# Optimization experiments

Measured on AMD Instinct MI355X. Metric: run time of the kernel, lower is better.

## Reference

```python
import jax, jax.numpy as jnp
import numpy as np

N_NODES = 50000
N_EDGES = 800000
D_IN = 128
D_OUT = 128


def setup_inputs() -> dict:
    key = jax.random.key(0)
    ks = jax.random.split(key, 10)
    x = jax.random.normal(ks[0], (N_NODES, D_IN), dtype=jnp.float32)
    lp_rows = jax.random.randint(ks[1], (N_EDGES,), 0, N_NODES, dtype=jnp.int32)
    lp_cols = jax.random.randint(ks[2], (N_EDGES,), 0, N_NODES, dtype=jnp.int32)
    # low-pass operator: positive normalized-adjacency-like weights
    lp_vals = jax.random.uniform(ks[3], (N_EDGES,), dtype=jnp.float32) / 16.0
    hp_rows = jax.random.randint(ks[4], (N_EDGES,), 0, N_NODES, dtype=jnp.int32)
    hp_cols = jax.random.randint(ks[5], (N_EDGES,), 0, N_NODES, dtype=jnp.int32)
    # high-pass operator: signed (Laplacian-like) weights
    hp_vals = jax.random.normal(ks[6], (N_EDGES,), dtype=jnp.float32) / 16.0
    alpha_w = jax.random.normal(ks[7], (1, D_IN), dtype=jnp.float32) * 0.05
    alpha_b = jnp.zeros((1,), dtype=jnp.float32)
    W = jax.random.normal(ks[8], (D_OUT, D_IN), dtype=jnp.float32) * (1.0 / np.sqrt(D_IN))
    b = jnp.zeros((D_OUT,), dtype=jnp.float32)
    return {"x": x, "lp_rows": lp_rows, "lp_cols": lp_cols, "lp_vals": lp_vals,
            "hp_rows": hp_rows, "hp_cols": hp_cols, "hp_vals": hp_vals,
            "alpha_w": alpha_w, "alpha_b": alpha_b, "W": W, "b": b}


def _spmm(rows, cols, vals, x, n):
    # COO sparse-dense matmul: out[r] += vals[e] * x[cols[e]]
    return jax.ops.segment_sum(vals[:, None] * x[cols], rows, num_segments=n)


def reference(x, lp_rows, lp_cols, lp_vals, hp_rows, hp_cols, hp_vals,
              alpha_w, alpha_b, W, b):
    n = x.shape[0]
    # per-node mixing gate: alpha_i = sigmoid(x_i . theta + b)  -> [N, 1]
    alpha = jax.nn.sigmoid(x @ alpha_w.T + alpha_b)
    z_lp = _spmm(lp_rows, lp_cols, lp_vals, x, n)   # [N, D_IN]
    z_hp = _spmm(hp_rows, hp_cols, hp_vals, x, n)   # [N, D_IN]
    z_mix = alpha * z_lp + (1.0 - alpha) * z_hp
    out = jax.nn.relu(z_mix @ W.T + b)              # use_activation=True
    return out, alpha
```

## Files before the change

kernel.cpp:

```cpp
#include <hip/hip_runtime.h>

#define N_NODES_C 50000
#define N_EDGES_C 800000
#define N_EDGES2_C (2 * N_EDGES_C)
#define D 128
#define CAP 128

static __device__ __forceinline__ unsigned short f2bf(float f) {
  unsigned u = __float_as_uint(f);
  u += 0x7fff + ((u >> 16) & 1);
  return (unsigned short)(u >> 16);
}
static __device__ __forceinline__ float bf_lo(unsigned u) {
  return __uint_as_float(u << 16);
}
static __device__ __forceinline__ float bf_hi(unsigned u) {
  return __uint_as_float(u & 0xffff0000u);
}

__global__ __launch_bounds__(256) void alpha_kernel(
    const float* __restrict__ x,
    const float* __restrict__ aw,
    const float* __restrict__ ab,
    float* __restrict__ alpha_out,
    float* __restrict__ alpha_ws,
    int n) {
  int wave = (int)((blockIdx.x * blockDim.x + threadIdx.x) >> 6);
  int lane = threadIdx.x & 63;
  if (wave >= n) return;
  const float* xr = x + (size_t)wave * D;
  float s = xr[lane] * aw[lane] + xr[lane + 64] * aw[lane + 64];
  #pragma unroll
  for (int off = 32; off > 0; off >>= 1)
    s += __shfl_down(s, off);
  if (lane == 0) {
    float a = 1.0f / (1.0f + __expf(-(s + ab[0])));
    alpha_out[wave] = a;
    alpha_ws[wave] = a;
  }
}

__global__ __launch_bounds__(256) void fill_kernel(
    const int* __restrict__ lp_rows, const int* __restrict__ lp_cols,
    const float* __restrict__ lp_vals,
    const int* __restrict__ hp_rows, const int* __restrict__ hp_cols,
    const float* __restrict__ hp_vals,
    const float* __restrict__ alpha,
    int* __restrict__ rcursor,
    unsigned* __restrict__ pairs) {
  int e = blockIdx.x * 256 + threadIdx.x;
  if (e >= N_EDGES2_C) return;
  int r, c;
  float v;
  if (e < N_EDGES_C) {
    r = lp_rows[e];
    c = lp_cols[e];
    v = lp_vals[e] * alpha[r];
  } else {
    int i = e - N_EDGES_C;
    r = hp_rows[i];
    c = hp_cols[i];
    v = hp_vals[i] * (1.0f - alpha[r]);
  }
  unsigned pk = (unsigned)c | ((unsigned)f2bf(v) << 16);
  int p = atomicAdd(&rcursor[r], 1);
  if (p < CAP) pairs[((size_t)r << 7) + p] = pk;
}

#define GNODES 64
#define GP 16
#define LDP 132

__global__ __launch_bounds__(256) void gemm_y_kernel(
    const float* __restrict__ x,
    const float* __restrict__ W,
    unsigned* __restrict__ y,
    int n) {
  __shared__ float wt[D][LDP];
  __shared__ float zs[GP][LDP];

  int t = threadIdx.x;
  int node0 = blockIdx.x * GNODES;

  #pragma unroll
  for (int it = 0; it < 16; ++it) {
    int f = t + it * 256;
    int j = f >> 5;
    int k4 = f & 31;
    *(float4*)&wt[j][k4 * 4] = ((const float4*)W)[f];
  }

  int tj = t & 31;
  int ns = t >> 5;
  int j0 = tj * 2;

  for (int p = 0; p < 4; ++p) {
    int nb = node0 + p * GP;
    __syncthreads();
    #pragma unroll
    for (int it = 0; it < 2; ++it) {
      int f = t + it * 256;
      int r = f >> 5;
      int c4 = f & 31;
      int node = nb + r;
      float4 v = make_float4(0.f, 0.f, 0.f, 0.f);
      if (node < n) v = ((const float4*)(x + (size_t)node * D))[c4];
      *(float4*)&zs[r][c4 * 4] = v;
    }
    __syncthreads();

    float acc[2][4] = {};
    #pragma unroll 4
    for (int k = 0; k < D; k += 4) {
      float4 w0 = *(const float4*)&wt[j0][k];
      float4 w1 = *(const float4*)&wt[j0 + 1][k];
      float4 w2 = *(const float4*)&wt[j0 + 64][k];
      float4 w3 = *(const float4*)&wt[j0 + 65][k];
      float4 z0 = *(const float4*)&zs[ns * 2 + 0][k];
      float4 z1 = *(const float4*)&zs[ns * 2 + 1][k];
      acc[0][0] += z0.x * w0.x + z0.y * w0.y + z0.z * w0.z + z0.w * w0.w;
      acc[0][1] += z0.x * w1.x + z0.y * w1.y + z0.z * w1.z + z0.w * w1.w;
      acc[0][2] += z0.x * w2.x + z0.y * w2.y + z0.z * w2.z + z0.w * w2.w;
      acc[0][3] += z0.x * w3.x + z0.y * w3.y + z0.z * w3.z + z0.w * w3.w;
      acc[1][0] += z1.x * w0.x + z1.y * w0.y + z1.z * w0.z + z1.w * w0.w;
      acc[1][1] += z1.x * w1.x + z1.y * w1.y + z1.z * w1.z + z1.w * w1.w;
      acc[1][2] += z1.x * w2.x + z1.y * w2.y + z1.z * w2.z + z1.w * w2.w;
      acc[1][3] += z1.x * w3.x + z1.y * w3.y + z1.z * w3.z + z1.w * w3.w;
    }

    #pragma unroll
    for (int ii = 0; ii < 2; ++ii) {
      int node = nb + ns * 2 + ii;
      if (node < n) {
        uint2 o;
        o.x = (unsigned)f2bf(acc[ii][0]) | ((unsigned)f2bf(acc[ii][2]) << 16);
        o.y = (unsigned)f2bf(acc[ii][1]) | ((unsigned)f2bf(acc[ii][3]) << 16);
        *(uint2*)&y[(size_t)node * 64 + j0] = o;
      }
    }
  }
}

__global__ __launch_bounds__(256) void gather_kernel(
    const int* __restrict__ rcursor,
    const unsigned* __restrict__ pairs,
    const unsigned* __restrict__ y,
    const float* __restrict__ bias,
    float* __restrict__ out) {
  int row = (int)((blockIdx.x * blockDim.x + threadIdx.x) >> 6);
  int lane = threadIdx.x & 63;
  if (row >= N_NODES_C) return;
  int deg = rcursor[row];
  if (deg > CAP) deg = CAP;
  const unsigned* pp = pairs + ((size_t)row << 7);
  float aL = 0.f, aH = 0.f;
  int p = 0;
  for (; p + 3 < deg; p += 4) {
    unsigned e0 = pp[p + 0];
    unsigned e1 = pp[p + 1];
    unsigned e2 = pp[p + 2];
    unsigned e3 = pp[p + 3];
    unsigned u0 = y[(size_t)(e0 & 0xffffu) * 64 + lane];
    unsigned u1 = y[(size_t)(e1 & 0xffffu) * 64 + lane];
    unsigned u2 = y[(size_t)(e2 & 0xffffu) * 64 + lane];
    unsigned u3 = y[(size_t)(e3 & 0xffffu) * 64 + lane];
    float v0 = bf_hi(e0);
    float v1 = bf_hi(e1);
    float v2 = bf_hi(e2);
    float v3 = bf_hi(e3);
    aL += v0 * bf_lo(u0) + v1 * bf_lo(u1) + v2 * bf_lo(u2) + v3 * bf_lo(u3);
    aH += v0 * bf_hi(u0) + v1 * bf_hi(u1) + v2 * bf_hi(u2) + v3 * bf_hi(u3);
  }
  for (; p < deg; ++p) {
    unsigned e0 = pp[p];
    unsigned u0 = y[(size_t)(e0 & 0xffffu) * 64 + lane];
    float v0 = bf_hi(e0);
    aL += v0 * bf_lo(u0);
    aH += v0 * bf_hi(u0);
  }
  out[(size_t)row * D + lane] = fmaxf(aL + bias[lane], 0.0f);
  out[(size_t)row * D + lane + 64] = fmaxf(aH + bias[lane + 64], 0.0f);
}

extern "C" void kernel_launch(void* const* d_in, const int* in_sizes, int n_in,
                              void* d_out, int out_size, void* d_ws, size_t ws_size,
                              hipStream_t stream) {
  const float* x = (const float*)d_in[0];
  const int* lp_rows = (const int*)d_in[1];
  const int* lp_cols = (const int*)d_in[2];
  const float* lp_vals = (const float*)d_in[3];
  const int* hp_rows = (const int*)d_in[4];
  const int* hp_cols = (const int*)d_in[5];
  const float* hp_vals = (const float*)d_in[6];
  const float* alpha_w = (const float*)d_in[7];
  const float* alpha_b = (const float*)d_in[8];
  const float* W = (const float*)d_in[9];
  const float* bias = (const float*)d_in[10];

  float* out = (float*)d_out;
  float* alpha_out = out + (size_t)N_NODES_C * D;

  char* ws = (char*)d_ws;
  unsigned* y = (unsigned*)ws;           ws += (size_t)N_NODES_C * 64 * 4;
  float* alpha_ws = (float*)ws;          ws += 200192;
  int* rcursor = (int*)ws;               ws += 200192;
  unsigned* pairs = (unsigned*)ws;
  ws += (size_t)N_NODES_C * CAP * 4;

  hipMemsetAsync(rcursor, 0, N_NODES_C * sizeof(int), stream);

  alpha_kernel<<<(N_NODES_C + 3) / 4, 256, 0, stream>>>(
      x, alpha_w, alpha_b, alpha_out, alpha_ws, N_NODES_C);

  fill_kernel<<<(N_EDGES2_C + 255) / 256, 256, 0, stream>>>(
      lp_rows, lp_cols, lp_vals, hp_rows, hp_cols, hp_vals,
      alpha_ws, rcursor, pairs);

  gemm_y_kernel<<<(N_NODES_C + GNODES - 1) / GNODES, 256, 0, stream>>>(
      x, W, y, N_NODES_C);

  gather_kernel<<<(N_NODES_C * 64 + 255) / 256, 256, 0, stream>>>(
      rcursor, pairs, (const unsigned*)y, bias, out);
}
```

Measured before the change: 307.6 us.

## Shard per-row edge buckets by XCD to localize atomic counters

The fill kernel now keeps eight per-row cursors and bucket segments, one per XCD, chosen by reading the hardware XCC id. The goal is to keep atomicAdd traffic on each row's counter within a single XCD's L2 and avoid cross-die coherence contention. The gather kernel walks all eight shards per row, adding loop overhead and doubling the pairs buffer footprint. Each shard holds at most 32 entries, so a heavily skewed distribution within one row could drop edges where the old 128-entry cap would not have.

```diff
diff --git a/kernel.cpp b/kernel.cpp
--- a/kernel.cpp
+++ b/kernel.cpp
@@ -4,7 +4,8 @@
 #define N_EDGES_C 800000
 #define N_EDGES2_C (2 * N_EDGES_C)
 #define D 128
-#define CAP 128
+#define NSHARD 8
+#define SCAP 32
 
 static __device__ __forceinline__ unsigned short f2bf(float f) {
   unsigned u = __float_as_uint(f);
@@ -16,6 +17,12 @@
 }
 static __device__ __forceinline__ float bf_hi(unsigned u) {
   return __uint_as_float(u & 0xffff0000u);
+}
+
+static __device__ __forceinline__ int xcd_id() {
+  int v;
+  asm volatile("s_getreg_b32 %0, hwreg(HW_REG_XCC_ID, 0, 4)" : "=s"(v));
+  return v & (NSHARD - 1);
 }
 
 __global__ __launch_bounds__(256) void alpha_kernel(
@@ -50,6 +57,7 @@
     unsigned* __restrict__ pairs) {
   int e = blockIdx.x * 256 + threadIdx.x;
   if (e >= N_EDGES2_C) return;
+  int xcc = xcd_id();
   int r, c;
   float v;
   if (e < N_EDGES_C) {
@@ -63,8 +71,8 @@
     v = hp_vals[i] * (1.0f - alpha[r]);
   }
   unsigned pk = (unsigned)c | ((unsigned)f2bf(v) << 16);
-  int p = atomicAdd(&rcursor[r], 1);
-  if (p < CAP) pairs[((size_t)r << 7) + p] = pk;
+  int p = atomicAdd(&rcursor[(r << 3) + xcc], 1);
+  if (p < SCAP) pairs[((size_t)r << 8) + (xcc << 5) + p] = pk;
 }
 
 #define GNODES 64
@@ -150,33 +158,38 @@
   int row = (int)((blockIdx.x * blockDim.x + threadIdx.x) >> 6);
   int lane = threadIdx.x & 63;
   if (row >= N_NODES_C) return;
-  int deg = rcursor[row];
-  if (deg > CAP) deg = CAP;
-  const unsigned* pp = pairs + ((size_t)row << 7);
+  const unsigned* pp = pairs + ((size_t)row << 8);
+  const int* cc = rcursor + (row << 3);
   float aL = 0.f, aH = 0.f;
-  int p = 0;
-  for (; p + 3 < deg; p += 4) {
-    unsigned e0 = pp[p + 0];
-    unsigned e1 = pp[p + 1];
-    unsigned e2 = pp[p + 2];
-    unsigned e3 = pp[p + 3];
-    unsigned u0 = y[(size_t)(e0 & 0xffffu) * 64 + lane];
-    unsigned u1 = y[(size_t)(e1 & 0xffffu) * 64 + lane];
-    unsigned u2 = y[(size_t)(e2 & 0xffffu) * 64 + lane];
-    unsigned u3 = y[(size_t)(e3 & 0xffffu) * 64 + lane];
-    float v0 = bf_hi(e0);
-    float v1 = bf_hi(e1);
-    float v2 = bf_hi(e2);
-    float v3 = bf_hi(e3);
-    aL += v0 * bf_lo(u0) + v1 * bf_lo(u1) + v2 * bf_lo(u2) + v3 * bf_lo(u3);
-    aH += v0 * bf_hi(u0) + v1 * bf_hi(u1) + v2 * bf_hi(u2) + v3 * bf_hi(u3);
-  }
-  for (; p < deg; ++p) {
-    unsigned e0 = pp[p];
-    unsigned u0 = y[(size_t)(e0 & 0xffffu) * 64 + lane];
-    float v0 = bf_hi(e0);
-    aL += v0 * bf_lo(u0);
-    aH += v0 * bf_hi(u0);
+  #pragma unroll
+  for (int s = 0; s < NSHARD; ++s) {
+    int deg = cc[s];
+    if (deg > SCAP) deg = SCAP;
+    const unsigned* cp = pp + (s << 5);
+    int p = 0;
+    for (; p + 3 < deg; p += 4) {
+      unsigned e0 = cp[p + 0];
+      unsigned e1 = cp[p + 1];
+      unsigned e2 = cp[p + 2];
+      unsigned e3 = cp[p + 3];
+      unsigned u0 = y[(size_t)(e0 & 0xffffu) * 64 + lane];
+      unsigned u1 = y[(size_t)(e1 & 0xffffu) * 64 + lane];
+      unsigned u2 = y[(size_t)(e2 & 0xffffu) * 64 + lane];
+      unsigned u3 = y[(size_t)(e3 & 0xffffu) * 64 + lane];
+      float v0 = bf_hi(e0);
+      float v1 = bf_hi(e1);
+      float v2 = bf_hi(e2);
+      float v3 = bf_hi(e3);
+      aL += v0 * bf_lo(u0) + v1 * bf_lo(u1) + v2 * bf_lo(u2) + v3 * bf_lo(u3);
+      aH += v0 * bf_hi(u0) + v1 * bf_hi(u1) + v2 * bf_hi(u2) + v3 * bf_hi(u3);
+    }
+    for (; p < deg; ++p) {
+      unsigned e0 = cp[p];
+      unsigned u0 = y[(size_t)(e0 & 0xffffu) * 64 + lane];
+      float v0 = bf_hi(e0);
+      aL += v0 * bf_lo(u0);
+      aH += v0 * bf_hi(u0);
+    }
   }
   out[(size_t)row * D + lane] = fmaxf(aL + bias[lane], 0.0f);
   out[(size_t)row * D + lane + 64] = fmaxf(aH + bias[lane + 64], 0.0f);
@@ -203,11 +216,11 @@
   char* ws = (char*)d_ws;
   unsigned* y = (unsigned*)ws;           ws += (size_t)N_NODES_C * 64 * 4;
   float* alpha_ws = (float*)ws;          ws += 200192;
-  int* rcursor = (int*)ws;               ws += 200192;
+  int* rcursor = (int*)ws;               ws += (size_t)N_NODES_C * NSHARD * 4;
   unsigned* pairs = (unsigned*)ws;
-  ws += (size_t)N_NODES_C * CAP * 4;
-
-  hipMemsetAsync(rcursor, 0, N_NODES_C * sizeof(int), stream);
+  ws += (size_t)N_NODES_C * NSHARD * SCAP * 4;
+
+  hipMemsetAsync(rcursor, 0, (size_t)N_NODES_C * NSHARD * sizeof(int), stream);
 
   alpha_kernel<<<(N_NODES_C + 3) / 4, 256, 0, stream>>>(
       x, alpha_w, alpha_b, alpha_out, alpha_ws, N_NODES_C);
```

After: 343.7 us. +11.7%, slower.
